# Kernel optimization log

Hardware: AMD Instinct MI355X
Metric: run time of the kernel (lower is better)

The kernel has to match this reference:

```python
import jax, jax.numpy as jnp
import numpy as np

DIM = 768
HEADS = 12
HEAD_DIM = DIM // HEADS
B, N = 8, 1024


def setup_inputs() -> dict:
    key = jax.random.key(0)
    ks = jax.random.split(key, 5)
    x = jax.random.normal(ks[0], (B, N, DIM), dtype=jnp.float32)
    shared_rel_pos = jax.random.normal(ks[1], (HEADS, N, N), dtype=jnp.float32)
    qkv_w = jax.random.normal(ks[2], (3 * DIM, DIM), dtype=jnp.float32) * (DIM ** -0.5)
    proj_w = jax.random.normal(ks[3], (DIM, DIM), dtype=jnp.float32) * (DIM ** -0.5)
    proj_b = jnp.zeros((DIM,), dtype=jnp.float32)
    return {"x": x, "shared_rel_pos": shared_rel_pos, "qkv_w": qkv_w,
            "proj_w": proj_w, "proj_b": proj_b}


def reference(x, shared_rel_pos, qkv_w, proj_w, proj_b):
    Bt, Nt, C = x.shape
    scale = HEAD_DIM ** -0.5
    # qkv: Linear(dim, 3*dim, bias=False) -> (B, N, 3, H, hd) -> (3, B, H, N, hd)
    qkv = jnp.einsum('bnc,oc->bno', x, qkv_w)
    qkv = qkv.reshape(Bt, Nt, 3, HEADS, HEAD_DIM).transpose(2, 0, 3, 1, 4)
    q, k, v = qkv[0], qkv[1], qkv[2]
    # scaled dot-product attention with shared relative-position bias
    attn = jnp.einsum('bhqd,bhkd->bhqk', q, k) * scale
    attn = attn + shared_rel_pos[None]  # broadcast over batch
    attn = jax.nn.softmax(attn, axis=-1)
    out = jnp.einsum('bhqk,bhkd->bhqd', attn, v)
    out = out.transpose(0, 2, 1, 3).reshape(Bt, Nt, C)
    return jnp.einsum('bnc,oc->bno', out, proj_w) + proj_b
```

## Files before the change

### kernel.cpp

```cpp
#include <hip/hip_runtime.h>
#include <hip/hip_bf16.h>
#include <stdint.h>

#define HEADS 12
#define HD 64
#define SEQ 1024
#define CDIM 768
#define LOG2E 1.44269504f

typedef __attribute__((ext_vector_type(8))) short bfrag;
typedef __attribute__((ext_vector_type(4))) float facc;
typedef __attribute__((ext_vector_type(4))) _Float16 h4;
typedef __attribute__((ext_vector_type(2))) __fp16 pk2;

__device__ __forceinline__ ushort f2bf(float f) {
    union { float f; uint32_t u; } v; v.f = f;
    uint32_t u = v.u;
    uint32_t r = (u + 0x7FFFu + ((u >> 16) & 1u)) >> 16;
    return (ushort)r;
}
__device__ __forceinline__ ushort f2h(float f) {
    union { _Float16 h; ushort u; } c; c.h = (_Float16)f; return c.u;
}
__device__ __forceinline__ float h2f(uint32_t u16) {
    union { _Float16 h; ushort u; } c; c.u = (ushort)u16; return (float)c.h;
}
__device__ __forceinline__ h4 pack4h(float p0, float p1, float p2, float p3) {
    union { h4 v4; pk2 v2[2]; } u;
    u.v2[0] = __builtin_amdgcn_cvt_pkrtz(p0, p1);
    u.v2[1] = __builtin_amdgcn_cvt_pkrtz(p2, p3);
    return u.v4;
}
__device__ __forceinline__ float exp2_raw(float x) {
    float r;
    asm("v_exp_f32 %0, %1" : "=v"(r) : "v"(x));
    return r;
}

__global__ void cvt_all(const float* __restrict__ x, const float* __restrict__ qw,
                        const float* __restrict__ pw,
                        ushort* __restrict__ xd, ushort* __restrict__ qd,
                        ushort* __restrict__ pd) {
    long i = ((long)blockIdx.x * 256 + threadIdx.x) * 4;
    if (i < 6291456) {
        float4 v = *(const float4*)(x + i);
        ushort4 o = {f2bf(v.x), f2bf(v.y), f2bf(v.z), f2bf(v.w)};
        *(ushort4*)(xd + i) = o;
    } else if (i < 8060928) {
        long j = i - 6291456;
        float4 v = *(const float4*)(qw + j);
        ushort4 o = {f2bf(v.x), f2bf(v.y), f2bf(v.z), f2bf(v.w)};
        *(ushort4*)(qd + j) = o;
    } else if (i < 8650752) {
        long j = i - 8060928;
        float4 v = *(const float4*)(pw + j);
        ushort4 o = {f2bf(v.x), f2bf(v.y), f2bf(v.z), f2bf(v.w)};
        *(ushort4*)(pd + j) = o;
    }
}

#define GLOAD16(gsrc, ldst) \
    __builtin_amdgcn_global_load_lds((const __attribute__((address_space(1))) uint32_t*)(gsrc), \
                                     (__attribute__((address_space(3))) uint32_t*)(ldst), 16, 0, 0)

template<int EPI>
__global__ __launch_bounds__(256) void gemm_nt(
    const ushort* __restrict__ A, const ushort* __restrict__ Bm,
    ushort* __restrict__ qb, ushort* __restrict__ kb, ushort* __restrict__ vb,
    const float* __restrict__ projb, float* __restrict__ out,
    const float* __restrict__ relf, ushort* __restrict__ biash)
{
    __shared__ ushort As[128 * 64];
    __shared__ ushort Bs[128 * 64];
    const int t = threadIdx.x;

    int m0, o0;
    if (EPI == 0) {
        if (blockIdx.y < 4) {
            const int cb = blockIdx.y * 64 + blockIdx.x;
#pragma unroll 4
            for (int s = 0; s < 48; ++s) {
                long i = (((long)s * 256 + cb) * 256 + t) * 4;
                float4 v = *(const float4*)(relf + i);
                ushort4 o = {f2h(v.x * LOG2E), f2h(v.y * LOG2E),
                             f2h(v.z * LOG2E), f2h(v.w * LOG2E)};
                *(ushort4*)(biash + i) = o;
            }
            return;
        }
        m0 = blockIdx.x * 128;
        o0 = (blockIdx.y - 4) * 128;
    } else {
        m0 = blockIdx.x * 128;
        o0 = blockIdx.y * 128;
    }

    const int w = t >> 6, l = t & 63;
    const int wm = w >> 1, wn = w & 1;
    const int lr = l & 15, lg = l >> 4;

    facc acc[4][4] = {};

    const int srow = w * 8 + (l >> 3);
    const int sgr  = ((l & 7) ^ (l >> 3)) * 8;
    const ushort* Ag = A + (size_t)(m0 + srow) * CDIM + sgr;
    const ushort* Bg = Bm + (size_t)(o0 + srow) * CDIM + sgr;
    const int ldst = w * 512 + l * 8;

    for (int k0 = 0; k0 < CDIM; k0 += 64) {
        __syncthreads();
#pragma unroll
        for (int j = 0; j < 4; ++j) {
            GLOAD16(Ag + (size_t)(j * 32) * CDIM + k0, As + j * 2048 + ldst);
            GLOAD16(Bg + (size_t)(j * 32) * CDIM + k0, Bs + j * 2048 + ldst);
        }
        __syncthreads();
#pragma unroll
        for (int s = 0; s < 2; ++s) {
            bfrag af[4], bf[4];
            const int rg = ((s * 4 + lg) ^ (lr & 7)) * 8;
#pragma unroll
            for (int m = 0; m < 4; ++m)
                af[m] = *(const bfrag*)&As[(wm * 64 + m * 16 + lr) * 64 + rg];
#pragma unroll
            for (int n = 0; n < 4; ++n)
                bf[n] = *(const bfrag*)&Bs[(wn * 64 + n * 16 + lr) * 64 + rg];
#pragma unroll
            for (int m = 0; m < 4; ++m)
#pragma unroll
                for (int n = 0; n < 4; ++n)
                    acc[m][n] = __builtin_amdgcn_mfma_f32_16x16x32_bf16(af[m], bf[n], acc[m][n], 0, 0, 0);
        }
    }

    if (EPI == 0) {
        const int tsel = o0 / CDIM;
        const int h_base = (o0 % CDIM) / 64;
        if (tsel == 2) {
#pragma unroll
            for (int m = 0; m < 4; ++m) {
                int grow = m0 + wm * 64 + m * 16 + lg * 4;
                int b = grow >> 10, nn = grow & 1023;
#pragma unroll
                for (int n = 0; n < 4; ++n) {
                    int h = h_base + wn;
                    int d = n * 16 + lr;
                    ushort4 pk = {f2h(acc[m][n][0]), f2h(acc[m][n][1]),
                                  f2h(acc[m][n][2]), f2h(acc[m][n][3])};
                    *(ushort4*)&vb[(((size_t)(b * HEADS + h)) * 64 + d) * 1024 + nn] = pk;
                }
            }
        } else {
            ushort* dst = (tsel == 0) ? qb : kb;
            const float scl = (tsel == 0) ? 0.18033688f : 1.0f;
#pragma unroll
            for (int m = 0; m < 4; ++m) {
                int grow = m0 + wm * 64 + m * 16 + lg * 4;
#pragma unroll
                for (int n = 0; n < 4; ++n) {
                    int h = h_base + wn;
                    int d = n * 16 + lr;
#pragma unroll
                    for (int r = 0; r < 4; ++r) {
                        int row = grow + r;
                        int b = row >> 10, nn = row & 1023;
                        dst[(((size_t)(b * HEADS + h)) * SEQ + nn) * HD + d] = f2bf(acc[m][n][r] * scl);
                    }
                }
            }
        }
    } else {
#pragma unroll
        for (int m = 0; m < 4; ++m) {
            int grow = m0 + wm * 64 + m * 16 + lg * 4;
#pragma unroll
            for (int n = 0; n < 4; ++n) {
                int o = o0 + wn * 64 + n * 16 + lr;
                float bias = projb[o];
#pragma unroll
                for (int r = 0; r < 4; ++r)
                    out[(size_t)(grow + r) * CDIM + o] = acc[m][n][r] + bias;
            }
        }
    }
}

__global__ __launch_bounds__(256, 3) void attn_kernel(
    const ushort* __restrict__ qbuf, const ushort* __restrict__ kbuf,
    const ushort* __restrict__ vtbuf, const ushort* __restrict__ biash,
    ushort* __restrict__ attn_out)
{
    __shared__ ushort Ks[2][64 * 64];
    __shared__ ushort Vt[2][64 * 64];

    const int t = threadIdx.x;
    const int w = t >> 6, l = t & 63;
    const int lr = l & 15, lg = l >> 4;

    const int bid = blockIdx.x;
    const int lid = (bid & 7) * 96 + (bid >> 3);
    const int h  = lid >> 6;
    const int qt = (lid >> 3) & 7;
    const int b  = lid & 7;

    const int q0 = qt * 128;
    const size_t headoff = (size_t)(b * HEADS + h) * SEQ * HD;
    const int qrb = q0 + w * 32;

    bfrag aQ[2][2];
#pragma unroll
    for (int n = 0; n < 2; ++n) {
        const ushort* Qp = qbuf + headoff + (size_t)(qrb + n * 16 + lr) * HD;
        aQ[n][0] = *(const bfrag*)(Qp + lg * 8);
        aQ[n][1] = *(const bfrag*)(Qp + 32 + lg * 8);
    }

    float mrun[2] = {-1e30f, -1e30f};
    float lrun[2] = {0.0f, 0.0f};
    facc Ov[2][4] = {};

    const ushort* bprow[2];
#pragma unroll
    for (int n = 0; n < 2; ++n)
        bprow[n] = biash + ((size_t)h * SEQ + qrb + n * 16 + lr) * SEQ;

    const ushort* kbh  = kbuf  + headoff;
    const ushort* vtbh = vtbuf + (size_t)(b * HEADS + h) * 65536;
    const int srow = (w << 3) + (l >> 3);
    const int sgr  = ((l & 7) ^ (srow & 7)) << 3;

    const int g0 = (lg ^ (lr & 7)) << 3;

    GLOAD16(kbh + (size_t)srow * 64 + sgr,            &Ks[0][w * 512]);
    GLOAD16(kbh + (size_t)(srow + 32) * 64 + sgr,     &Ks[0][2048 + w * 512]);
    GLOAD16(vtbh + (size_t)srow * 1024 + sgr,         &Vt[0][w * 512]);
    GLOAD16(vtbh + (size_t)(srow + 32) * 1024 + sgr,  &Vt[0][2048 + w * 512]);
    uint2 bcur[2][4];
#pragma unroll
    for (int n = 0; n < 2; ++n)
#pragma unroll
        for (int c = 0; c < 4; ++c)
            bcur[n][c] = *(const uint2*)(bprow[n] + c * 16 + lg * 4);
    __syncthreads();

    for (int tt = 0; tt < 16; ++tt) {
        const int cur = tt & 1;
        const ushort* Kc = Ks[cur];
        const ushort* Vc = Vt[cur];

        if (tt < 15) {
            const int kvn = (tt + 1) << 6;
            GLOAD16(kbh + (size_t)(kvn + srow) * 64 + sgr,           &Ks[cur ^ 1][w * 512]);
            GLOAD16(kbh + (size_t)(kvn + srow + 32) * 64 + sgr,      &Ks[cur ^ 1][2048 + w * 512]);
            GLOAD16(vtbh + (size_t)srow * 1024 + kvn + sgr,          &Vt[cur ^ 1][w * 512]);
            GLOAD16(vtbh + (size_t)(srow + 32) * 1024 + kvn + sgr,   &Vt[cur ^ 1][2048 + w * 512]);
        }

        facc St[2][4];
        h4 pf[2][4];
        float psum[2] = {0.0f, 0.0f};
        float pmax[2] = {-3.0e38f, -3.0e38f};
#pragma unroll
        for (int c = 0; c < 4; ++c) {
            bfrag kf0 = *(const bfrag*)&Kc[(c * 16 + lr) * 64 + g0];
            bfrag kf1 = *(const bfrag*)&Kc[(c * 16 + lr) * 64 + (g0 ^ 32)];
#pragma unroll
            for (int n = 0; n < 2; ++n) {
                uint2 bb = bcur[n][c];
                facc s;
                s[0] = h2f(bb.x & 0xffffu);
                s[1] = h2f(bb.x >> 16);
                s[2] = h2f(bb.y & 0xffffu);
                s[3] = h2f(bb.y >> 16);
                __builtin_amdgcn_s_setprio(1);
                s = __builtin_amdgcn_mfma_f32_16x16x32_bf16(kf0, aQ[n][0], s, 0, 0, 0);
                s = __builtin_amdgcn_mfma_f32_16x16x32_bf16(kf1, aQ[n][1], s, 0, 0, 0);
                __builtin_amdgcn_s_setprio(0);
                St[n][c] = s;
                float p0 = exp2_raw(s[0] - mrun[n]);
                float p1 = exp2_raw(s[1] - mrun[n]);
                float p2f = exp2_raw(s[2] - mrun[n]);
                float p3 = exp2_raw(s[3] - mrun[n]);
                psum[n] += (p0 + p1) + (p2f + p3);
                pmax[n] = fmaxf(pmax[n], fmaxf(fmaxf(s[0], s[1]), fmaxf(s[2], s[3])));
                pf[n][c] = pack4h(p0, p1, p2f, p3);
            }
        }

        if (tt < 15) {
            const int kvn = (tt + 1) << 6;
#pragma unroll
            for (int n = 0; n < 2; ++n)
#pragma unroll
                for (int c = 0; c < 4; ++c)
                    bcur[n][c] = *(const uint2*)(bprow[n] + kvn + c * 16 + lg * 4);
        }

        int viol = (pmax[0] > mrun[0] + 14.0f) || (pmax[1] > mrun[1] + 14.0f);
        if (__any(viol)) {
#pragma unroll
            for (int n = 0; n < 2; ++n) {
                float pm = pmax[n];
                pm = fmaxf(pm, __shfl_xor(pm, 16));
                pm = fmaxf(pm, __shfl_xor(pm, 32));
                float mnew = fmaxf(mrun[n], pm);
                float al = exp2_raw(mrun[n] - mnew);
                psum[n] = 0.0f;
#pragma unroll
                for (int c = 0; c < 4; ++c) {
                    float p0 = exp2_raw(St[n][c][0] - mnew);
                    float p1 = exp2_raw(St[n][c][1] - mnew);
                    float p2f = exp2_raw(St[n][c][2] - mnew);
                    float p3 = exp2_raw(St[n][c][3] - mnew);
                    psum[n] += (p0 + p1) + (p2f + p3);
                    pf[n][c] = pack4h(p0, p1, p2f, p3);
                }
#pragma unroll
                for (int r = 0; r < 4; ++r) {
                    float a = __shfl(al, lg * 4 + r);
#pragma unroll
                    for (int d = 0; d < 4; ++d) Ov[n][d][r] *= a;
                }
                lrun[n] *= al;
                mrun[n] = mnew;
            }
        }

        __builtin_amdgcn_s_setprio(1);
#pragma unroll
        for (int c = 0; c < 4; ++c) {
#pragma unroll
            for (int d0 = 0; d0 < 4; ++d0) {
                int row = d0 * 16 + lr;
                h4 bv = *(const h4*)&Vc[row * 64 + ((((c * 2 + (lg >> 1)) ^ (lr & 7)) << 3) + ((lg & 1) << 2))];
#pragma unroll
                for (int n = 0; n < 2; ++n)
                    Ov[n][d0] = __builtin_amdgcn_mfma_f32_16x16x16f16(pf[n][c], bv, Ov[n][d0], 0, 0, 0);
            }
        }
        __builtin_amdgcn_s_setprio(0);

        lrun[0] += psum[0];
        lrun[1] += psum[1];

        if (tt < 15) __syncthreads();
    }

#pragma unroll
    for (int n = 0; n < 2; ++n) {
        float lt = lrun[n];
        lt += __shfl_xor(lt, 16);
        lt += __shfl_xor(lt, 32);
        ushort* op = attn_out + ((size_t)b * SEQ + qrb + n * 16) * CDIM + h * HD;
#pragma unroll
        for (int r = 0; r < 4; ++r) {
            float ll = __shfl(lt, lg * 4 + r);
            float rl = 1.0f / ll;
#pragma unroll
            for (int d = 0; d < 4; ++d)
                op[(size_t)(lg * 4 + r) * CDIM + d * 16 + lr] = f2bf(Ov[n][d][r] * rl);
        }
    }
}

extern "C" void kernel_launch(void* const* d_in, const int* in_sizes, int n_in,
                              void* d_out, int out_size, void* d_ws, size_t ws_size,
                              hipStream_t stream) {
    const float* x     = (const float*)d_in[0];
    const float* rel   = (const float*)d_in[1];
    const float* qkvw  = (const float*)d_in[2];
    const float* projw = (const float*)d_in[3];
    const float* projb = (const float*)d_in[4];
    float* out = (float*)d_out;

    char* ws = (char*)d_ws;
    ushort* biash = (ushort*)(ws);
    ushort* qb    = (ushort*)(ws + 25165824);
    ushort* kb    = (ushort*)(ws + 37748736);
    ushort* vb    = (ushort*)(ws + 50331648);
    ushort* attnb = (ushort*)(ws + 62914560);
    ushort* xbf   = attnb;
    ushort* wbf   = (ushort*)(ws + 75497472);
    ushort* pwbf  = (ushort*)(ws + 79036416);

    cvt_all<<<8448, 256, 0, stream>>>(x, qkvw, projw, xbf, wbf, pwbf);

    gemm_nt<0><<<dim3(64, 22), 256, 0, stream>>>(xbf, wbf, qb, kb, vb, nullptr, nullptr, rel, biash);
    attn_kernel<<<768, 256, 0, stream>>>(qb, kb, vb, biash, attnb);
    gemm_nt<1><<<dim3(64, 6), 256, 0, stream>>>(attnb, pwbf, nullptr, nullptr, nullptr, projb, out, nullptr, nullptr);
}
```

Measured before the change: 139.5 us.

## Halve attention query tile to 64 rows, doubling blocks and occupancy

Each attention wave now handles 16 query rows instead of 32, so a block covers 64 queries and the grid grows from 768 to 1536 blocks. The launch bound rises to 4 blocks per CU to match the smaller register footprint. The aim is more waves in flight to hide latency and better CU fill. In exchange, each K/V tile loaded into LDS is reused by half as many queries, so K/V global and LDS traffic roughly doubles.

```diff
diff --git a/kernel.cpp b/kernel.cpp
--- a/kernel.cpp
+++ b/kernel.cpp
@@ -185,7 +185,7 @@
     }
 }
 
-__global__ __launch_bounds__(256, 3) void attn_kernel(
+__global__ __launch_bounds__(256, 4) void attn_kernel(
     const ushort* __restrict__ qbuf, const ushort* __restrict__ kbuf,
     const ushort* __restrict__ vtbuf, const ushort* __restrict__ biash,
     ushort* __restrict__ attn_out)
@@ -198,31 +198,27 @@
     const int lr = l & 15, lg = l >> 4;
 
     const int bid = blockIdx.x;
-    const int lid = (bid & 7) * 96 + (bid >> 3);
-    const int h  = lid >> 6;
-    const int qt = (lid >> 3) & 7;
+    const int lid = (bid & 7) * 192 + (bid >> 3);
+    const int h  = lid >> 7;
+    const int qt = (lid >> 3) & 15;
     const int b  = lid & 7;
 
-    const int q0 = qt * 128;
+    const int q0 = qt * 64;
     const size_t headoff = (size_t)(b * HEADS + h) * SEQ * HD;
-    const int qrb = q0 + w * 32;
-
-    bfrag aQ[2][2];
-#pragma unroll
-    for (int n = 0; n < 2; ++n) {
-        const ushort* Qp = qbuf + headoff + (size_t)(qrb + n * 16 + lr) * HD;
-        aQ[n][0] = *(const bfrag*)(Qp + lg * 8);
-        aQ[n][1] = *(const bfrag*)(Qp + 32 + lg * 8);
-    }
-
-    float mrun[2] = {-1e30f, -1e30f};
-    float lrun[2] = {0.0f, 0.0f};
-    facc Ov[2][4] = {};
-
-    const ushort* bprow[2];
-#pragma unroll
-    for (int n = 0; n < 2; ++n)
-        bprow[n] = biash + ((size_t)h * SEQ + qrb + n * 16 + lr) * SEQ;
+    const int qrb = q0 + w * 16;
+
+    bfrag aQ0, aQ1;
+    {
+        const ushort* Qp = qbuf + headoff + (size_t)(qrb + lr) * HD;
+        aQ0 = *(const bfrag*)(Qp + lg * 8);
+        aQ1 = *(const bfrag*)(Qp + 32 + lg * 8);
+    }
+
+    float mrun = -1e30f;
+    float lrun = 0.0f;
+    facc Ov[4] = {};
+
+    const ushort* bprow = biash + ((size_t)h * SEQ + qrb + lr) * SEQ;
 
     const ushort* kbh  = kbuf  + headoff;
     const ushort* vtbh = vtbuf + (size_t)(b * HEADS + h) * 65536;
@@ -235,12 +231,10 @@
     GLOAD16(kbh + (size_t)(srow + 32) * 64 + sgr,     &Ks[0][2048 + w * 512]);
     GLOAD16(vtbh + (size_t)srow * 1024 + sgr,         &Vt[0][w * 512]);
     GLOAD16(vtbh + (size_t)(srow + 32) * 1024 + sgr,  &Vt[0][2048 + w * 512]);
-    uint2 bcur[2][4];
-#pragma unroll
-    for (int n = 0; n < 2; ++n)
-#pragma unroll
-        for (int c = 0; c < 4; ++c)
-            bcur[n][c] = *(const uint2*)(bprow[n] + c * 16 + lg * 4);
+    uint2 bcur[4];
+#pragma unroll
+    for (int c = 0; c < 4; ++c)
+        bcur[c] = *(const uint2*)(bprow + c * 16 + lg * 4);
     __syncthreads();
 
     for (int tt = 0; tt < 16; ++tt) {
@@ -256,74 +250,64 @@
             GLOAD16(vtbh + (size_t)(srow + 32) * 1024 + kvn + sgr,   &Vt[cur ^ 1][2048 + w * 512]);
         }
 
-        facc St[2][4];
-        h4 pf[2][4];
-        float psum[2] = {0.0f, 0.0f};
-        float pmax[2] = {-3.0e38f, -3.0e38f};
+        facc St[4];
+        h4 pf[4];
+        float psum = 0.0f, pmax = -3.0e38f;
 #pragma unroll
         for (int c = 0; c < 4; ++c) {
             bfrag kf0 = *(const bfrag*)&Kc[(c * 16 + lr) * 64 + g0];
             bfrag kf1 = *(const bfrag*)&Kc[(c * 16 + lr) * 64 + (g0 ^ 32)];
-#pragma unroll
-            for (int n = 0; n < 2; ++n) {
-                uint2 bb = bcur[n][c];
-                facc s;
-                s[0] = h2f(bb.x & 0xffffu);
-                s[1] = h2f(bb.x >> 16);
-                s[2] = h2f(bb.y & 0xffffu);
-                s[3] = h2f(bb.y >> 16);
-                __builtin_amdgcn_s_setprio(1);
-                s = __builtin_amdgcn_mfma_f32_16x16x32_bf16(kf0, aQ[n][0], s, 0, 0, 0);
-                s = __builtin_amdgcn_mfma_f32_16x16x32_bf16(kf1, aQ[n][1], s, 0, 0, 0);
-                __builtin_amdgcn_s_setprio(0);
-                St[n][c] = s;
-                float p0 = exp2_raw(s[0] - mrun[n]);
-                float p1 = exp2_raw(s[1] - mrun[n]);
-                float p2f = exp2_raw(s[2] - mrun[n]);
-                float p3 = exp2_raw(s[3] - mrun[n]);
-                psum[n] += (p0 + p1) + (p2f + p3);
-                pmax[n] = fmaxf(pmax[n], fmaxf(fmaxf(s[0], s[1]), fmaxf(s[2], s[3])));
-                pf[n][c] = pack4h(p0, p1, p2f, p3);
-            }
+            uint2 bb = bcur[c];
+            facc s;
+            s[0] = h2f(bb.x & 0xffffu);
+            s[1] = h2f(bb.x >> 16);
+            s[2] = h2f(bb.y & 0xffffu);
+            s[3] = h2f(bb.y >> 16);
+            __builtin_amdgcn_s_setprio(1);
+            s = __builtin_amdgcn_mfma_f32_16x16x32_bf16(kf0, aQ0, s, 0, 0, 0);
+            s = __builtin_amdgcn_mfma_f32_16x16x32_bf16(kf1, aQ1, s, 0, 0, 0);
+            __builtin_amdgcn_s_setprio(0);
+            St[c] = s;
+            float p0 = exp2_raw(s[0] - mrun);
+            float p1 = exp2_raw(s[1] - mrun);
+            float p2f = exp2_raw(s[2] - mrun);
+            float p3 = exp2_raw(s[3] - mrun);
+            psum += (p0 + p1) + (p2f + p3);
+            pmax = fmaxf(pmax, fmaxf(fmaxf(s[0], s[1]), fmaxf(s[2], s[3])));
+            pf[c] = pack4h(p0, p1, p2f, p3);
         }
 
         if (tt < 15) {
             const int kvn = (tt + 1) << 6;
 #pragma unroll
-            for (int n = 0; n < 2; ++n)
-#pragma unroll
-                for (int c = 0; c < 4; ++c)
-                    bcur[n][c] = *(const uint2*)(bprow[n] + kvn + c * 16 + lg * 4);
-        }
-
-        int viol = (pmax[0] > mrun[0] + 14.0f) || (pmax[1] > mrun[1] + 14.0f);
-        if (__any(viol)) {
-#pragma unroll
-            for (int n = 0; n < 2; ++n) {
-                float pm = pmax[n];
-                pm = fmaxf(pm, __shfl_xor(pm, 16));
-                pm = fmaxf(pm, __shfl_xor(pm, 32));
-                float mnew = fmaxf(mrun[n], pm);
-                float al = exp2_raw(mrun[n] - mnew);
-                psum[n] = 0.0f;
-#pragma unroll
-                for (int c = 0; c < 4; ++c) {
-                    float p0 = exp2_raw(St[n][c][0] - mnew);
-                    float p1 = exp2_raw(St[n][c][1] - mnew);
-                    float p2f = exp2_raw(St[n][c][2] - mnew);
-                    float p3 = exp2_raw(St[n][c][3] - mnew);
-                    psum[n] += (p0 + p1) + (p2f + p3);
-                    pf[n][c] = pack4h(p0, p1, p2f, p3);
-                }
-#pragma unroll
-                for (int r = 0; r < 4; ++r) {
-                    float a = __shfl(al, lg * 4 + r);
-#pragma unroll
-                    for (int d = 0; d < 4; ++d) Ov[n][d][r] *= a;
-                }
-                lrun[n] *= al;
-                mrun[n] = mnew;
-            }
+            for (int c = 0; c < 4; ++c)
+                bcur[c] = *(const uint2*)(bprow + kvn + c * 16 + lg * 4);
+        }
+
+        if (__any(pmax > mrun + 14.0f)) {
+            float pm = pmax;
+            pm = fmaxf(pm, __shfl_xor(pm, 16));
+            pm = fmaxf(pm, __shfl_xor(pm, 32));
+            float mnew = fmaxf(mrun, pm);
+            float al = exp2_raw(mrun - mnew);
+            psum = 0.0f;
+#pragma unroll
+            for (int c = 0; c < 4; ++c) {
+                float p0 = exp2_raw(St[c][0] - mnew);
+                float p1 = exp2_raw(St[c][1] - mnew);
+                float p2f = exp2_raw(St[c][2] - mnew);
+                float p3 = exp2_raw(St[c][3] - mnew);
+                psum += (p0 + p1) + (p2f + p3);
+                pf[c] = pack4h(p0, p1, p2f, p3);
+            }
+#pragma unroll
+            for (int r = 0; r < 4; ++r) {
+                float a = __shfl(al, lg * 4 + r);
+#pragma unroll
+                for (int d = 0; d < 4; ++d) Ov[d][r] *= a;
+            }
+            lrun *= al;
+            mrun = mnew;
         }
 
         __builtin_amdgcn_s_setprio(1);
@@ -333,33 +317,27 @@
             for (int d0 = 0; d0 < 4; ++d0) {
                 int row = d0 * 16 + lr;
                 h4 bv = *(const h4*)&Vc[row * 64 + ((((c * 2 + (lg >> 1)) ^ (lr & 7)) << 3) + ((lg & 1) << 2))];
-#pragma unroll
-                for (int n = 0; n < 2; ++n)
-                    Ov[n][d0] = __builtin_amdgcn_mfma_f32_16x16x16f16(pf[n][c], bv, Ov[n][d0], 0, 0, 0);
+                Ov[d0] = __builtin_amdgcn_mfma_f32_16x16x16f16(pf[c], bv, Ov[d0], 0, 0, 0);
             }
         }
         __builtin_amdgcn_s_setprio(0);
 
-        lrun[0] += psum[0];
-        lrun[1] += psum[1];
+        lrun += psum;
 
         if (tt < 15) __syncthreads();
     }
 
-#pragma unroll
-    for (int n = 0; n < 2; ++n) {
-        float lt = lrun[n];
-        lt += __shfl_xor(lt, 16);
-        lt += __shfl_xor(lt, 32);
-        ushort* op = attn_out + ((size_t)b * SEQ + qrb + n * 16) * CDIM + h * HD;
-#pragma unroll
-        for (int r = 0; r < 4; ++r) {
-            float ll = __shfl(lt, lg * 4 + r);
-            float rl = 1.0f / ll;
-#pragma unroll
-            for (int d = 0; d < 4; ++d)
-                op[(size_t)(lg * 4 + r) * CDIM + d * 16 + lr] = f2bf(Ov[n][d][r] * rl);
-        }
+    float lt = lrun;
+    lt += __shfl_xor(lt, 16);
+    lt += __shfl_xor(lt, 32);
+    ushort* op = attn_out + ((size_t)b * SEQ + qrb) * CDIM + h * HD;
+#pragma unroll
+    for (int r = 0; r < 4; ++r) {
+        float ll = __shfl(lt, lg * 4 + r);
+        float rl = 1.0f / ll;
+#pragma unroll
+        for (int d = 0; d < 4; ++d)
+            op[(size_t)(lg * 4 + r) * CDIM + d * 16 + lr] = f2bf(Ov[d][r] * rl);
     }
 }
 
@@ -386,6 +364,6 @@
     cvt_all<<<8448, 256, 0, stream>>>(x, qkvw, projw, xbf, wbf, pwbf);
 
     gemm_nt<0><<<dim3(64, 22), 256, 0, stream>>>(xbf, wbf, qb, kb, vb, nullptr, nullptr, rel, biash);
-    attn_kernel<<<768, 256, 0, stream>>>(qb, kb, vb, biash, attnb);
+    attn_kernel<<<1536, 256, 0, stream>>>(qb, kb, vb, biash, attnb);
     gemm_nt<1><<<dim3(64, 6), 256, 0, stream>>>(attnb, pwbf, nullptr, nullptr, nullptr, projb, out, nullptr, nullptr);
 }
```

Measured after the change: 145.0 us. +3.9%, slower.
